# Optimization experiments

Measured on AMD Instinct MI355X. Metric: run time of the kernel, lower is better.

Reference implementation:

```python
import jax, jax.numpy as jnp
import numpy as np

N_NODES = 20000
N_EDGES = 150000


def _nnconv(x, src, dst, edge_attr, nn_W, nn_b, root, bias, in_c, out_c):
    # Edge-conditioned conv (PyG NNConv, aggr='add'):
    #   W_e = edge_nn(edge_attr_e).reshape(in_c, out_c)
    #   out_i = sum_{e: dst(e)=i} x_{src(e)} @ W_e + x_i @ root + bias
    E = edge_attr.shape[0]
    W = (edge_attr @ nn_W.T + nn_b).reshape(E, in_c, out_c)  # [E, in_c, out_c]
    xj = x[src]                                              # gather [E, in_c]
    msg = jnp.einsum('ei,eio->eo', xj, W)                    # per-edge matmul
    aggr = jax.ops.segment_sum(msg, dst, num_segments=x.shape[0])
    return aggr + x @ root + bias


def setup_inputs() -> dict:
    key = jax.random.key(0)
    ks = jax.random.split(key, 20)

    def glorot(k, shape):
        fan = sum(shape)
        return jax.random.normal(k, shape, dtype=jnp.float32) * jnp.sqrt(2.0 / fan)

    x = jax.random.normal(ks[0], (N_NODES, 2), dtype=jnp.float32)
    edge_index = jax.random.randint(ks[1], (2, N_EDGES), 0, N_NODES, dtype=jnp.int64)
    edge_attr = jax.random.normal(ks[2], (N_EDGES, 2), dtype=jnp.float32)

    return {
        'x': x, 'edge_index': edge_index, 'edge_attr': edge_attr,
        # conv1: in=2, out=32, edge-net Linear(2, 64)
        'nn1_W': glorot(ks[3], (64, 2)), 'nn1_b': jnp.zeros((64,), jnp.float32),
        'root1': glorot(ks[4], (2, 32)), 'b1': jnp.zeros((32,), jnp.float32),
        # conv2: in=32, out=32, edge-net Linear(2, 1024)
        'nn2_W': glorot(ks[5], (1024, 2)), 'nn2_b': jnp.zeros((1024,), jnp.float32),
        'root2': glorot(ks[6], (32, 32)), 'b2': jnp.zeros((32,), jnp.float32),
        # conv3: in=32, out=32, edge-net Linear(2, 1024)
        'nn3_W': glorot(ks[7], (1024, 2)), 'nn3_b': jnp.zeros((1024,), jnp.float32),
        'root3': glorot(ks[8], (32, 32)), 'b3': jnp.zeros((32,), jnp.float32),
        # dense head
        'fc1_W': glorot(ks[9], (32, 32)), 'fc1_b': jnp.zeros((32,), jnp.float32),
        'fc2_W': glorot(ks[10], (1, 32)), 'fc2_b': jnp.zeros((1,), jnp.float32),
    }


def reference(x, edge_index, edge_attr,
              nn1_W, nn1_b, root1, b1,
              nn2_W, nn2_b, root2, b2,
              nn3_W, nn3_b, root3, b3,
              fc1_W, fc1_b, fc2_W, fc2_b):
    src, dst = edge_index[0], edge_index[1]
    h = jax.nn.relu(_nnconv(x, src, dst, edge_attr, nn1_W, nn1_b, root1, b1, 2, 32))
    h = jax.nn.relu(_nnconv(h, src, dst, edge_attr, nn2_W, nn2_b, root2, b2, 32, 32))
    h = jax.nn.relu(_nnconv(h, src, dst, edge_attr, nn3_W, nn3_b, root3, b3, 32, 32))
    h = jax.nn.relu(h @ fc1_W.T + fc1_b)
    return h @ fc2_W.T + fc2_b  # [N_NODES, 1]
```

## Files before the change

### kernel.cpp

```cpp
#include <hip/hip_runtime.h>


#define CAP 32

typedef float f32x4 __attribute__((ext_vector_type(4)));
typedef short s16x8 __attribute__((ext_vector_type(8)));

__device__ __forceinline__ unsigned short f2bf(float x) {
    unsigned u = __float_as_uint(x);
    unsigned r = u + 0x7FFFu + ((u >> 16) & 1u);
    return (unsigned short)(r >> 16);
}
__device__ __forceinline__ float bf2f(unsigned short h) {
    return __uint_as_float(((unsigned)h) << 16);
}

__global__ __launch_bounds__(256) void zero_kernel(int4* p, int n4) {
    int i = blockIdx.x * 256 + threadIdx.x;
    int gt = gridDim.x * 256;
    int4 z = {0, 0, 0, 0};
    for (; i < n4; i += gt) p[i] = z;
}

__global__ __launch_bounds__(256) void scatter_kernel(
    const int* __restrict__ src, const int* __restrict__ dst,
    const float* __restrict__ ea, int* __restrict__ cnt,
    int4* __restrict__ edges, int E) {
    int tid = blockIdx.x * 256 + threadIdx.x;
    int T = gridDim.x * 256;
#pragma unroll 4
    for (int k = 0; k < 4; ++k) {
        int e = tid + k * T;
        if (e < E) {
            int d = dst[e];
            int p = atomicAdd(&cnt[d], 1);
            if (p < CAP) {
                float2 a = ((const float2*)ea)[e];
                int4 ed;
                ed.x = __float_as_int(1.0f);
                ed.y = __float_as_int(a.x);
                ed.z = __float_as_int(a.y);
                ed.w = src[e] * 32;
                edges[((size_t)d << 5) + p] = ed;
            }
        }
    }
}

__global__ __launch_bounds__(256) void conv1_kernel(
    const float* __restrict__ x, const int* __restrict__ cnt,
    const int4* __restrict__ edges, const float* __restrict__ nnW,
    const float* __restrict__ nnb, const float* __restrict__ root,
    const float* __restrict__ bias, float* __restrict__ hout, int N) {
    int tid = threadIdx.x;
    int g = tid >> 5, lane = tid & 31;
    int n = blockIdx.x * 8 + g;
    if (n >= N) return;
    int deg = cnt[n];
    deg = (deg < CAP) ? deg : CAP;
    int deg4 = (deg + 3) & ~3;
    const int4* ep = &edges[(size_t)n << 5];
    float p0 = 0, p1 = 0, q0 = 0, q1 = 0, r0 = 0, r1 = 0;
    for (int p = 0; p < deg4; p += 4) {
        int4 e0 = ep[p], e1 = ep[p + 1], e2 = ep[p + 2], e3 = ep[p + 3];
        float2 x0 = ((const float2*)x)[e0.w >> 5];
        float2 x1 = ((const float2*)x)[e1.w >> 5];
        float2 x2 = ((const float2*)x)[e2.w >> 5];
        float2 x3 = ((const float2*)x)[e3.w >> 5];
        float w0 = __int_as_float(e0.x), w1 = __int_as_float(e1.x);
        float w2 = __int_as_float(e2.x), w3 = __int_as_float(e3.x);
        p0 = fmaf(__int_as_float(e0.y), x0.x, p0);
        p1 = fmaf(__int_as_float(e0.y), x0.y, p1);
        q0 = fmaf(__int_as_float(e0.z), x0.x, q0);
        q1 = fmaf(__int_as_float(e0.z), x0.y, q1);
        r0 = fmaf(w0, x0.x, r0); r1 = fmaf(w0, x0.y, r1);
        p0 = fmaf(__int_as_float(e1.y), x1.x, p0);
        p1 = fmaf(__int_as_float(e1.y), x1.y, p1);
        q0 = fmaf(__int_as_float(e1.z), x1.x, q0);
        q1 = fmaf(__int_as_float(e1.z), x1.y, q1);
        r0 = fmaf(w1, x1.x, r0); r1 = fmaf(w1, x1.y, r1);
        p0 = fmaf(__int_as_float(e2.y), x2.x, p0);
        p1 = fmaf(__int_as_float(e2.y), x2.y, p1);
        q0 = fmaf(__int_as_float(e2.z), x2.x, q0);
        q1 = fmaf(__int_as_float(e2.z), x2.y, q1);
        r0 = fmaf(w2, x2.x, r0); r1 = fmaf(w2, x2.y, r1);
        p0 = fmaf(__int_as_float(e3.y), x3.x, p0);
        p1 = fmaf(__int_as_float(e3.y), x3.y, p1);
        q0 = fmaf(__int_as_float(e3.z), x3.x, q0);
        q1 = fmaf(__int_as_float(e3.z), x3.y, q1);
        r0 = fmaf(w3, x3.x, r0); r1 = fmaf(w3, x3.y, r1);
    }
    float acc = bias[lane];
    acc = fmaf(p0, nnW[lane * 2], acc);
    acc = fmaf(p1, nnW[(32 + lane) * 2], acc);
    acc = fmaf(q0, nnW[lane * 2 + 1], acc);
    acc = fmaf(q1, nnW[(32 + lane) * 2 + 1], acc);
    acc = fmaf(r0, nnb[lane], acc);
    acc = fmaf(r1, nnb[32 + lane], acc);
    float2 xn = ((const float2*)x)[n];
    acc = fmaf(xn.x, root[lane], acc);
    acc = fmaf(xn.y, root[32 + lane], acc);
    hout[n * 32 + lane] = fmaxf(acc, 0.f);
}

template <int BS>
__device__ __forceinline__ void stage_weights(
    const float* __restrict__ nnW, const float* __restrict__ nnb,
    const float* __restrict__ root, unsigned short (*Whi)[32][32],
    unsigned short (*Wlo)[32][32], int t) {
    for (int idx = t; idx < 4096; idx += BS) {
        int kc = idx >> 10, r = idx & 1023, k = r >> 5, o = r & 31;
        float v = (kc == 0)   ? nnW[(k * 32 + o) * 2]
                  : (kc == 1) ? nnW[(k * 32 + o) * 2 + 1]
                  : (kc == 2) ? nnb[k * 32 + o]
                              : root[k * 32 + o];
        unsigned short hb = f2bf(v);
        Whi[kc][o][k] = hb;
        Wlo[kc][o][k] = f2bf(v - bf2f(hb));
    }
}

#define MFMA_BF16 __builtin_amdgcn_mfma_f32_16x16x32_bf16

__device__ __forceinline__ void gather_to_lds(
    const float* __restrict__ h, const int* __restrict__ cnt,
    const int4* __restrict__ edges, float (*Sl)[132], int base, int t, int N) {
    int g = t >> 5, lane = t & 31;
    int n = base + g;
    float s0 = 0, s1 = 0, s2 = 0, s3 = 0;
    if (n < N) {
        int deg = cnt[n];
        deg = (deg < CAP) ? deg : CAP;
        int deg4 = (deg + 3) & ~3;
        const int4* ep = &edges[(size_t)n << 5];
        s3 = h[n * 32 + lane];
        for (int p = 0; p < deg4; p += 4) {
            int4 e0 = ep[p], e1 = ep[p + 1], e2 = ep[p + 2], e3 = ep[p + 3];
            float h0 = h[e0.w + lane];
            float h1 = h[e1.w + lane];
            float h2 = h[e2.w + lane];
            float h3 = h[e3.w + lane];
            s0 = fmaf(__int_as_float(e0.y), h0, s0);
            s1 = fmaf(__int_as_float(e0.z), h0, s1);
            s2 = fmaf(__int_as_float(e0.x), h0, s2);
            s0 = fmaf(__int_as_float(e1.y), h1, s0);
            s1 = fmaf(__int_as_float(e1.z), h1, s1);
            s2 = fmaf(__int_as_float(e1.x), h1, s2);
            s0 = fmaf(__int_as_float(e2.y), h2, s0);
            s1 = fmaf(__int_as_float(e2.z), h2, s1);
            s2 = fmaf(__int_as_float(e2.x), h2, s2);
            s0 = fmaf(__int_as_float(e3.y), h3, s0);
            s1 = fmaf(__int_as_float(e3.z), h3, s1);
            s2 = fmaf(__int_as_float(e3.x), h3, s2);
        }
    }
    Sl[g][lane] = s0;
    Sl[g][32 + lane] = s1;
    Sl[g][64 + lane] = s2;
    Sl[g][96 + lane] = s3;
}

__device__ __forceinline__ void tile_mfma(
    const float (*Sl)[132], const unsigned short (*Whi)[32][32],
    const unsigned short (*Wlo)[32][32], int q, int c, f32x4* acc0, f32x4* acc1) {
#pragma unroll
    for (int kc = 0; kc < 4; ++kc) {
        const float* sp = &Sl[c][kc * 32 + q * 8];
        s16x8 ah, al;
#pragma unroll
        for (int e = 0; e < 8; ++e) {
            float v = sp[e];
            unsigned short hb = f2bf(v);
            ah[e] = (short)hb;
            al[e] = (short)f2bf(v - bf2f(hb));
        }
        s16x8 bh0 = *reinterpret_cast<const s16x8*>(&Whi[kc][c][q * 8]);
        s16x8 bl0 = *reinterpret_cast<const s16x8*>(&Wlo[kc][c][q * 8]);
        s16x8 bh1 = *reinterpret_cast<const s16x8*>(&Whi[kc][16 + c][q * 8]);
        s16x8 bl1 = *reinterpret_cast<const s16x8*>(&Wlo[kc][16 + c][q * 8]);
        *acc0 = MFMA_BF16(ah, bh0, *acc0, 0, 0, 0);
        *acc0 = MFMA_BF16(al, bh0, *acc0, 0, 0, 0);
        *acc0 = MFMA_BF16(ah, bl0, *acc0, 0, 0, 0);
        *acc1 = MFMA_BF16(ah, bh1, *acc1, 0, 0, 0);
        *acc1 = MFMA_BF16(al, bh1, *acc1, 0, 0, 0);
        *acc1 = MFMA_BF16(ah, bl1, *acc1, 0, 0, 0);
    }
}

__global__ __launch_bounds__(512) void fused2_kernel(
    const float* __restrict__ h, const int* __restrict__ cnt,
    const int4* __restrict__ edges, const float* __restrict__ nnW,
    const float* __restrict__ nnb, const float* __restrict__ root,
    const float* __restrict__ bias, float* __restrict__ hout, int N) {
    __shared__ unsigned short Whi[4][32][32], Wlo[4][32][32];
    __shared__ float Sl[16][132];
    int t = threadIdx.x;
    int base = blockIdx.x * 16;
    stage_weights<512>(nnW, nnb, root, Whi, Wlo, t);
    gather_to_lds(h, cnt, edges, Sl, base, t, N);
    __syncthreads();
    if (t < 64) {
        int q = t >> 4, c = t & 15;
        f32x4 acc0 = {0.f, 0.f, 0.f, 0.f}, acc1 = {0.f, 0.f, 0.f, 0.f};
        tile_mfma(Sl, Whi, Wlo, q, c, &acc0, &acc1);
        float bb0 = bias[c], bb1 = bias[16 + c];
#pragma unroll
        for (int rr = 0; rr < 4; ++rr) {
            int n = base + q * 4 + rr;
            if (n < N) {
                hout[(size_t)n * 32 + c] = fmaxf(acc0[rr] + bb0, 0.f);
                hout[(size_t)n * 32 + 16 + c] = fmaxf(acc1[rr] + bb1, 0.f);
            }
        }
    }
}

__global__ __launch_bounds__(512) void fused3_kernel(
    const float* __restrict__ h, const int* __restrict__ cnt,
    const int4* __restrict__ edges, const float* __restrict__ nnW,
    const float* __restrict__ nnb, const float* __restrict__ root,
    const float* __restrict__ bias, const float* __restrict__ fc1W,
    const float* __restrict__ fc1b, const float* __restrict__ fc2W,
    const float* __restrict__ fc2b, float* __restrict__ out, int N) {
    __shared__ unsigned short Whi[4][32][32], Wlo[4][32][32];
    __shared__ float Sl[16][132];
    __shared__ unsigned short Th[16][32], Tl[16][32];
    int t = threadIdx.x;
    int base = blockIdx.x * 16;
    stage_weights<512>(nnW, nnb, root, Whi, Wlo, t);
    gather_to_lds(h, cnt, edges, Sl, base, t, N);
    __syncthreads();
    int q = t >> 4, c = t & 15;
    if (t < 64) {
        f32x4 acc0 = {0.f, 0.f, 0.f, 0.f}, acc1 = {0.f, 0.f, 0.f, 0.f};
        tile_mfma(Sl, Whi, Wlo, q, c, &acc0, &acc1);
        float bb0 = bias[c], bb1 = bias[16 + c];
#pragma unroll
        for (int rr = 0; rr < 4; ++rr) {
            int row = q * 4 + rr;
            float v0 = fmaxf(acc0[rr] + bb0, 0.f);
            float v1 = fmaxf(acc1[rr] + bb1, 0.f);
            unsigned short hb;
            hb = f2bf(v0); Th[row][c] = hb;      Tl[row][c] = f2bf(v0 - bf2f(hb));
            hb = f2bf(v1); Th[row][16 + c] = hb; Tl[row][16 + c] = f2bf(v1 - bf2f(hb));
        }
    }
    __syncthreads();
    if (t < 64) {
        s16x8 fh[2], fl[2];
#pragma unroll
        for (int nc = 0; nc < 2; ++nc)
#pragma unroll
            for (int e = 0; e < 8; ++e) {
                float v = fc1W[(nc * 16 + c) * 32 + q * 8 + e];
                unsigned short hb = f2bf(v);
                fh[nc][e] = (short)hb;
                fl[nc][e] = (short)f2bf(v - bf2f(hb));
            }
        s16x8 hh = *reinterpret_cast<const s16x8*>(&Th[c][q * 8]);
        s16x8 hl = *reinterpret_cast<const s16x8*>(&Tl[c][q * 8]);
        f32x4 z0 = {0.f, 0.f, 0.f, 0.f}, z1 = {0.f, 0.f, 0.f, 0.f};
        z0 = MFMA_BF16(hh, fh[0], z0, 0, 0, 0);
        z0 = MFMA_BF16(hl, fh[0], z0, 0, 0, 0);
        z0 = MFMA_BF16(hh, fl[0], z0, 0, 0, 0);
        z1 = MFMA_BF16(hh, fh[1], z1, 0, 0, 0);
        z1 = MFMA_BF16(hl, fh[1], z1, 0, 0, 0);
        z1 = MFMA_BF16(hh, fl[1], z1, 0, 0, 0);
        float f1b0 = fc1b[c], f1b1 = fc1b[16 + c];
        float w20 = fc2W[c], w21 = fc2W[16 + c];
        float f2b = fc2b[0];
#pragma unroll
        for (int rr = 0; rr < 4; ++rr) {
            float zz0 = fmaxf(z0[rr] + f1b0, 0.f);
            float zz1 = fmaxf(z1[rr] + f1b1, 0.f);
            float v = fmaf(zz0, w20, zz1 * w21);
            v += __shfl_xor(v, 1);
            v += __shfl_xor(v, 2);
            v += __shfl_xor(v, 4);
            v += __shfl_xor(v, 8);
            int n = base + q * 4 + rr;
            if (c == 0 && n < N) out[n] = v + f2b;
        }
    }
}

static inline size_t align256(size_t v) { return (v + 255) & ~(size_t)255; }

extern "C" void kernel_launch(void* const* d_in, const int* in_sizes, int n_in,
                              void* d_out, int out_size, void* d_ws, size_t ws_size,
                              hipStream_t stream) {
    const float* x = (const float*)d_in[0];
    const int* ei = (const int*)d_in[1];
    const float* ea = (const float*)d_in[2];
    const float* nn1W = (const float*)d_in[3];
    const float* nn1b = (const float*)d_in[4];
    const float* root1 = (const float*)d_in[5];
    const float* b1 = (const float*)d_in[6];
    const float* nn2W = (const float*)d_in[7];
    const float* nn2b = (const float*)d_in[8];
    const float* root2 = (const float*)d_in[9];
    const float* b2 = (const float*)d_in[10];
    const float* nn3W = (const float*)d_in[11];
    const float* nn3b = (const float*)d_in[12];
    const float* root3 = (const float*)d_in[13];
    const float* b3 = (const float*)d_in[14];
    const float* fc1W = (const float*)d_in[15];
    const float* fc1b = (const float*)d_in[16];
    const float* fc2W = (const float*)d_in[17];
    const float* fc2b = (const float*)d_in[18];

    const int N = in_sizes[0] / 2;
    const int E = in_sizes[2] / 2;
    const int* src = ei;
    const int* dst = ei + E;

    char* w = (char*)d_ws;
    int* cnt = (int*)w;     w += align256((size_t)N * 4);
    int4* edges = (int4*)w; w += align256((size_t)N * CAP * 16);
    char* zero_end = w;
    float* h1 = (float*)w;  w += align256((size_t)N * 32 * 4);
    float* h2 = (float*)w;  w += align256((size_t)N * 32 * 4);

    float* out = (float*)d_out;

    int n4 = (int)((zero_end - (char*)cnt) / 16);
    zero_kernel<<<512, 256, 0, stream>>>((int4*)cnt, n4);

    int sb = (E + 1023) / 1024;
    scatter_kernel<<<sb, 256, 0, stream>>>(src, dst, ea, cnt, edges, E);

    int gb = (N + 7) / 8;
    int fb = (N + 15) / 16;
    conv1_kernel<<<gb, 256, 0, stream>>>(x, cnt, edges, nn1W, nn1b, root1, b1, h1, N);
    fused2_kernel<<<fb, 512, 0, stream>>>(h1, cnt, edges, nn2W, nn2b, root2, b2, h2, N);
    fused3_kernel<<<fb, 512, 0, stream>>>(h2, cnt, edges, nn3W, nn3b, root3, b3,
                                          fc1W, fc1b, fc2W, fc2b, out, N);
}
```

Before: 69.48 us.

## Split each node's edge list across two half-waves and reduce with shuffles

Each node is now handled by a full 64-lane wavefront instead of 32 lanes. The two halves each process half of the padded edge list and combine partial sums with a cross-half shuffle. This shortens the serial dependent-gather chain per node and raises memory-level parallelism. The cost is that each fused block now covers only 8 nodes, so the MFMA tiles are half padding and weight staging is repeated over twice as many blocks.

```diff
diff --git a/kernel.cpp b/kernel.cpp
--- a/kernel.cpp
+++ b/kernel.cpp
@@ -52,16 +52,20 @@
     const int4* __restrict__ edges, const float* __restrict__ nnW,
     const float* __restrict__ nnb, const float* __restrict__ root,
     const float* __restrict__ bias, float* __restrict__ hout, int N) {
-    int tid = threadIdx.x;
-    int g = tid >> 5, lane = tid & 31;
-    int n = blockIdx.x * 8 + g;
+    int t = threadIdx.x;
+    int wv = t >> 6, l = t & 63;
+    int half = l >> 5, lane = l & 31;
+    int n = blockIdx.x * 4 + wv;
     if (n >= N) return;
     int deg = cnt[n];
     deg = (deg < CAP) ? deg : CAP;
     int deg4 = (deg + 3) & ~3;
+    int c0 = ((deg4 >> 1) + 3) & ~3;
+    int pbeg = half ? c0 : 0;
+    int pend = half ? deg4 : c0;
     const int4* ep = &edges[(size_t)n << 5];
     float p0 = 0, p1 = 0, q0 = 0, q1 = 0, r0 = 0, r1 = 0;
-    for (int p = 0; p < deg4; p += 4) {
+    for (int p = pbeg; p < pend; p += 4) {
         int4 e0 = ep[p], e1 = ep[p + 1], e2 = ep[p + 2], e3 = ep[p + 3];
         float2 x0 = ((const float2*)x)[e0.w >> 5];
         float2 x1 = ((const float2*)x)[e1.w >> 5];
@@ -90,17 +94,25 @@
         q1 = fmaf(__int_as_float(e3.z), x3.y, q1);
         r0 = fmaf(w3, x3.x, r0); r1 = fmaf(w3, x3.y, r1);
     }
-    float acc = bias[lane];
-    acc = fmaf(p0, nnW[lane * 2], acc);
-    acc = fmaf(p1, nnW[(32 + lane) * 2], acc);
-    acc = fmaf(q0, nnW[lane * 2 + 1], acc);
-    acc = fmaf(q1, nnW[(32 + lane) * 2 + 1], acc);
-    acc = fmaf(r0, nnb[lane], acc);
-    acc = fmaf(r1, nnb[32 + lane], acc);
-    float2 xn = ((const float2*)x)[n];
-    acc = fmaf(xn.x, root[lane], acc);
-    acc = fmaf(xn.y, root[32 + lane], acc);
-    hout[n * 32 + lane] = fmaxf(acc, 0.f);
+    p0 += __shfl_xor(p0, 32);
+    p1 += __shfl_xor(p1, 32);
+    q0 += __shfl_xor(q0, 32);
+    q1 += __shfl_xor(q1, 32);
+    r0 += __shfl_xor(r0, 32);
+    r1 += __shfl_xor(r1, 32);
+    if (half == 0) {
+        float acc = bias[lane];
+        acc = fmaf(p0, nnW[lane * 2], acc);
+        acc = fmaf(p1, nnW[(32 + lane) * 2], acc);
+        acc = fmaf(q0, nnW[lane * 2 + 1], acc);
+        acc = fmaf(q1, nnW[(32 + lane) * 2 + 1], acc);
+        acc = fmaf(r0, nnb[lane], acc);
+        acc = fmaf(r1, nnb[32 + lane], acc);
+        float2 xn = ((const float2*)x)[n];
+        acc = fmaf(xn.x, root[lane], acc);
+        acc = fmaf(xn.y, root[32 + lane], acc);
+        hout[n * 32 + lane] = fmaxf(acc, 0.f);
+    }
 }
 
 template <int BS>
@@ -125,16 +137,20 @@
 __device__ __forceinline__ void gather_to_lds(
     const float* __restrict__ h, const int* __restrict__ cnt,
     const int4* __restrict__ edges, float (*Sl)[132], int base, int t, int N) {
-    int g = t >> 5, lane = t & 31;
-    int n = base + g;
+    int wv = t >> 6, l = t & 63;
+    int half = l >> 5, lane = l & 31;
+    int n = base + wv;
     float s0 = 0, s1 = 0, s2 = 0, s3 = 0;
     if (n < N) {
         int deg = cnt[n];
         deg = (deg < CAP) ? deg : CAP;
         int deg4 = (deg + 3) & ~3;
+        int c0 = ((deg4 >> 1) + 3) & ~3;
+        int pbeg = half ? c0 : 0;
+        int pend = half ? deg4 : c0;
         const int4* ep = &edges[(size_t)n << 5];
-        s3 = h[n * 32 + lane];
-        for (int p = 0; p < deg4; p += 4) {
+        if (half == 0) s3 = h[n * 32 + lane];
+        for (int p = pbeg; p < pend; p += 4) {
             int4 e0 = ep[p], e1 = ep[p + 1], e2 = ep[p + 2], e3 = ep[p + 3];
             float h0 = h[e0.w + lane];
             float h1 = h[e1.w + lane];
@@ -154,10 +170,15 @@
             s2 = fmaf(__int_as_float(e3.x), h3, s2);
         }
     }
-    Sl[g][lane] = s0;
-    Sl[g][32 + lane] = s1;
-    Sl[g][64 + lane] = s2;
-    Sl[g][96 + lane] = s3;
+    s0 += __shfl_xor(s0, 32);
+    s1 += __shfl_xor(s1, 32);
+    s2 += __shfl_xor(s2, 32);
+    if (half == 0) {
+        Sl[wv][lane] = s0;
+        Sl[wv][32 + lane] = s1;
+        Sl[wv][64 + lane] = s2;
+        Sl[wv][96 + lane] = s3;
+    }
 }
 
 __device__ __forceinline__ void tile_mfma(
@@ -195,7 +216,15 @@
     __shared__ unsigned short Whi[4][32][32], Wlo[4][32][32];
     __shared__ float Sl[16][132];
     int t = threadIdx.x;
-    int base = blockIdx.x * 16;
+    int base = blockIdx.x * 8;
+    if (t >= 256) {
+        int row = t >> 5;
+        int lane = t & 31;
+        Sl[row][lane] = 0.f;
+        Sl[row][32 + lane] = 0.f;
+        Sl[row][64 + lane] = 0.f;
+        Sl[row][96 + lane] = 0.f;
+    }
     stage_weights<512>(nnW, nnb, root, Whi, Wlo, t);
     gather_to_lds(h, cnt, edges, Sl, base, t, N);
     __syncthreads();
@@ -206,8 +235,9 @@
         float bb0 = bias[c], bb1 = bias[16 + c];
 #pragma unroll
         for (int rr = 0; rr < 4; ++rr) {
-            int n = base + q * 4 + rr;
-            if (n < N) {
+            int row = q * 4 + rr;
+            int n = base + row;
+            if (row < 8 && n < N) {
                 hout[(size_t)n * 32 + c] = fmaxf(acc0[rr] + bb0, 0.f);
                 hout[(size_t)n * 32 + 16 + c] = fmaxf(acc1[rr] + bb1, 0.f);
             }
@@ -226,7 +256,17 @@
     __shared__ float Sl[16][132];
     __shared__ unsigned short Th[16][32], Tl[16][32];
     int t = threadIdx.x;
-    int base = blockIdx.x * 16;
+    int base = blockIdx.x * 8;
+    if (t >= 256) {
+        int row = t >> 5;
+        int lane = t & 31;
+        Sl[row][lane] = 0.f;
+        Sl[row][32 + lane] = 0.f;
+        Sl[row][64 + lane] = 0.f;
+        Sl[row][96 + lane] = 0.f;
+        Th[row][lane] = 0;
+        Tl[row][lane] = 0;
+    }
     stage_weights<512>(nnW, nnb, root, Whi, Wlo, t);
     gather_to_lds(h, cnt, edges, Sl, base, t, N);
     __syncthreads();
@@ -238,11 +278,13 @@
 #pragma unroll
         for (int rr = 0; rr < 4; ++rr) {
             int row = q * 4 + rr;
-            float v0 = fmaxf(acc0[rr] + bb0, 0.f);
-            float v1 = fmaxf(acc1[rr] + bb1, 0.f);
-            unsigned short hb;
-            hb = f2bf(v0); Th[row][c] = hb;      Tl[row][c] = f2bf(v0 - bf2f(hb));
-            hb = f2bf(v1); Th[row][16 + c] = hb; Tl[row][16 + c] = f2bf(v1 - bf2f(hb));
+            if (row < 8) {
+                float v0 = fmaxf(acc0[rr] + bb0, 0.f);
+                float v1 = fmaxf(acc1[rr] + bb1, 0.f);
+                unsigned short hb;
+                hb = f2bf(v0); Th[row][c] = hb;      Tl[row][c] = f2bf(v0 - bf2f(hb));
+                hb = f2bf(v1); Th[row][16 + c] = hb; Tl[row][16 + c] = f2bf(v1 - bf2f(hb));
+            }
         }
     }
     __syncthreads();
@@ -271,6 +313,7 @@
         float f2b = fc2b[0];
 #pragma unroll
         for (int rr = 0; rr < 4; ++rr) {
+            int row = q * 4 + rr;
             float zz0 = fmaxf(z0[rr] + f1b0, 0.f);
             float zz1 = fmaxf(z1[rr] + f1b1, 0.f);
             float v = fmaf(zz0, w20, zz1 * w21);
@@ -278,8 +321,8 @@
             v += __shfl_xor(v, 2);
             v += __shfl_xor(v, 4);
             v += __shfl_xor(v, 8);
-            int n = base + q * 4 + rr;
-            if (c == 0 && n < N) out[n] = v + f2b;
+            int n = base + row;
+            if (c == 0 && row < 8 && n < N) out[n] = v + f2b;
         }
     }
 }
@@ -329,9 +372,9 @@
     int sb = (E + 1023) / 1024;
     scatter_kernel<<<sb, 256, 0, stream>>>(src, dst, ea, cnt, edges, E);
 
-    int gb = (N + 7) / 8;
-    int fb = (N + 15) / 16;
-    conv1_kernel<<<gb, 256, 0, stream>>>(x, cnt, edges, nn1W, nn1b, root1, b1, h1, N);
+    int cb = (N + 3) / 4;
+    int fb = (N + 7) / 8;
+    conv1_kernel<<<cb, 256, 0, stream>>>(x, cnt, edges, nn1W, nn1b, root1, b1, h1, N);
     fused2_kernel<<<fb, 512, 0, stream>>>(h1, cnt, edges, nn2W, nn2b, root2, b2, h2, N);
     fused3_kernel<<<fb, 512, 0, stream>>>(h2, cnt, edges, nn3W, nn3b, root3, b3,
                                           fc1W, fc1b, fc2W, fc2b, out, N);
```

Measured after the change: 90.11 us. 29.7% more time.
